# Kernel tuning notes

Hardware: AMD Instinct MI355X
Metric: run time of the kernel (lower is better)

Reference implementation:

```python
import jax, jax.numpy as jnp
import numpy as np


def setup_inputs() -> dict:
    key = jax.random.key(0)
    k1, k2, k3 = jax.random.split(key, 3)
    B, IN, OUT = 8192, 2048, 2048
    x = jax.random.normal(k1, (B, IN), dtype=jnp.float32)
    # kaiming_uniform_(a=sqrt(5)) on [OUT, IN] -> bound = sqrt(6/((1+5)*IN)) = 1/sqrt(IN)
    wb = 1.0 / np.sqrt(IN)
    weight = jax.random.uniform(k2, (OUT, IN), dtype=jnp.float32, minval=-wb, maxval=wb)
    bb = 1.0 / np.sqrt(IN)
    bias = jax.random.uniform(k3, (OUT,), dtype=jnp.float32, minval=-bb, maxval=bb)
    return {"x": x, "weight": weight, "bias": bias}


def reference(x, weight, bias):
    # out[b,o] = sum_i (x[b,i] + w[o,i]) = rowsum(x)[b] + rowsum(w)[o]
    # (identical math to the O(B*O*I) broadcast-sum, computed in O(B*I + O*I + B*O))
    x_sum = jnp.sum(x, axis=1)        # [B]
    w_sum = jnp.sum(weight, axis=1)   # [O]
    out = x_sum[:, None] + w_sum[None, :]  # [B, O]
    out = out * bias                  # note: original does `output *= self.bias`
    return out
```

## Files before the change

kernel.cpp:

```cpp
#include <hip/hip_runtime.h>


#define B_DIM 8192
#define IN_DIM 2048
#define OUT_DIM 2048

typedef float f32x4 __attribute__((ext_vector_type(4)));

__device__ __forceinline__ float butterfly_reduce(float s) {
    #pragma unroll
    for (int off = 32; off; off >>= 1)
        s += __shfl_xor(s, off, 64);
    return s;
}

__global__ __launch_bounds__(256) void wsb_kernel(const float* __restrict__ w,
                                                  const float* __restrict__ bias,
                                                  float* __restrict__ wsb) {
    const int wave = threadIdx.x >> 6;
    const int lane = threadIdx.x & 63;
    const int row  = (blockIdx.x << 2) + wave;
    const f32x4* src4 = reinterpret_cast<const f32x4*>(w + (size_t)row * IN_DIM);

    f32x4 v[8];
    #pragma unroll
    for (int k = 0; k < 8; ++k)
        v[k] = __builtin_nontemporal_load(&src4[lane + (k << 6)]);
    float s = 0.f;
    #pragma unroll
    for (int k = 0; k < 8; ++k)
        s += (v[k].x + v[k].y) + (v[k].z + v[k].w);
    s = butterfly_reduce(s);
    if (lane == 0)
        wsb[row] = s * bias[row];
}

__global__ __launch_bounds__(256) void fused_row_kernel(const float* __restrict__ x,
                                                        const float* __restrict__ bias,
                                                        const float* __restrict__ wsb,
                                                        f32x4* __restrict__ out4) {
    const int wave = threadIdx.x >> 6;
    const int lane = threadIdx.x & 63;
    const int row  = (blockIdx.x << 2) + wave;
    const f32x4* src4  = reinterpret_cast<const f32x4*>(x + (size_t)row * IN_DIM);
    const f32x4* bias4 = reinterpret_cast<const f32x4*>(bias);
    const f32x4* wsb4  = reinterpret_cast<const f32x4*>(wsb);

    f32x4 v[8];
    #pragma unroll
    for (int k = 0; k < 8; ++k)
        v[k] = __builtin_nontemporal_load(&src4[lane + (k << 6)]);
    float s = 0.f;
    #pragma unroll
    for (int k = 0; k < 8; ++k)
        s += (v[k].x + v[k].y) + (v[k].z + v[k].w);
    const float xs = butterfly_reduce(s);

    f32x4* orow = out4 + (size_t)row * (OUT_DIM / 4);
    #pragma unroll
    for (int k = 0; k < 8; ++k) {
        const int i = lane + (k << 6);
        const f32x4 bi = bias4[i];
        const f32x4 ws = wsb4[i];
        f32x4 o;
        o.x = fmaf(xs, bi.x, ws.x);
        o.y = fmaf(xs, bi.y, ws.y);
        o.z = fmaf(xs, bi.z, ws.z);
        o.w = fmaf(xs, bi.w, ws.w);
        __builtin_nontemporal_store(o, &orow[i]);
    }
}

extern "C" void kernel_launch(void* const* d_in, const int* in_sizes, int n_in,
                              void* d_out, int out_size, void* d_ws, size_t ws_size,
                              hipStream_t stream) {
    const float* x    = (const float*)d_in[0];
    const float* w    = (const float*)d_in[1];
    const float* bias = (const float*)d_in[2];
    float* out = (float*)d_out;
    float* wsb = (float*)d_ws;

    wsb_kernel<<<OUT_DIM / 4, 256, 0, stream>>>(w, bias, wsb);
    fused_row_kernel<<<B_DIM / 4, 256, 0, stream>>>(x, bias, wsb, (f32x4*)out);
}
```

Before: 32.99 us.

## Process four rows per wave with register double-buffered prefetch of next row

Each wave in the fused kernel now handles four consecutive x rows. It prefetches the next row into a second register buffer while it reduces the current row and writes that row's output, and the grid shrinks by a factor of four. The nontemporal load and store hints are also replaced with ordinary loads and stores in both kernels. The goal is to overlap load latency with compute and stores, and to reuse the bias and wsb reads. The cost is fewer waves to hide latency, more register pressure, and possibly worse cache behaviour without the nontemporal hints.

New measurement: 30.51 us. -7.5%, faster.

```diff
diff --git a/kernel.cpp b/kernel.cpp
--- a/kernel.cpp
+++ b/kernel.cpp
@@ -4,6 +4,7 @@
 #define B_DIM 8192
 #define IN_DIM 2048
 #define OUT_DIM 2048
+#define ROWS_PER_WAVE 4
 
 typedef float f32x4 __attribute__((ext_vector_type(4)));
 
@@ -14,23 +15,31 @@
     return s;
 }
 
+__device__ __forceinline__ void load_row(f32x4 (&v)[8], const float* __restrict__ row,
+                                         int lane) {
+    const f32x4* r4 = reinterpret_cast<const f32x4*>(row);
+    #pragma unroll
+    for (int k = 0; k < 8; ++k)
+        v[k] = r4[lane + (k << 6)];
+}
+
+__device__ __forceinline__ float reduce_row(const f32x4 (&v)[8]) {
+    float s = 0.f;
+    #pragma unroll
+    for (int k = 0; k < 8; ++k)
+        s += (v[k].x + v[k].y) + (v[k].z + v[k].w);
+    return butterfly_reduce(s);
+}
+
 __global__ __launch_bounds__(256) void wsb_kernel(const float* __restrict__ w,
                                                   const float* __restrict__ bias,
                                                   float* __restrict__ wsb) {
     const int wave = threadIdx.x >> 6;
     const int lane = threadIdx.x & 63;
     const int row  = (blockIdx.x << 2) + wave;
-    const f32x4* src4 = reinterpret_cast<const f32x4*>(w + (size_t)row * IN_DIM);
-
     f32x4 v[8];
-    #pragma unroll
-    for (int k = 0; k < 8; ++k)
-        v[k] = __builtin_nontemporal_load(&src4[lane + (k << 6)]);
-    float s = 0.f;
-    #pragma unroll
-    for (int k = 0; k < 8; ++k)
-        s += (v[k].x + v[k].y) + (v[k].z + v[k].w);
-    s = butterfly_reduce(s);
+    load_row(v, w + (size_t)row * IN_DIM, lane);
+    float s = reduce_row(v);
     if (lane == 0)
         wsb[row] = s * bias[row];
 }
@@ -41,33 +50,37 @@
                                                         f32x4* __restrict__ out4) {
     const int wave = threadIdx.x >> 6;
     const int lane = threadIdx.x & 63;
-    const int row  = (blockIdx.x << 2) + wave;
-    const f32x4* src4  = reinterpret_cast<const f32x4*>(x + (size_t)row * IN_DIM);
+    const int row0 = ((blockIdx.x << 2) + wave) * ROWS_PER_WAVE;
     const f32x4* bias4 = reinterpret_cast<const f32x4*>(bias);
     const f32x4* wsb4  = reinterpret_cast<const f32x4*>(wsb);
 
-    f32x4 v[8];
+    f32x4 cur[8], nxt[8];
+    load_row(cur, x + (size_t)row0 * IN_DIM, lane);
+
     #pragma unroll
-    for (int k = 0; k < 8; ++k)
-        v[k] = __builtin_nontemporal_load(&src4[lane + (k << 6)]);
-    float s = 0.f;
-    #pragma unroll
-    for (int k = 0; k < 8; ++k)
-        s += (v[k].x + v[k].y) + (v[k].z + v[k].w);
-    const float xs = butterfly_reduce(s);
+    for (int r = 0; r < ROWS_PER_WAVE; ++r) {
+        if (r + 1 < ROWS_PER_WAVE)
+            load_row(nxt, x + (size_t)(row0 + r + 1) * IN_DIM, lane);
 
-    f32x4* orow = out4 + (size_t)row * (OUT_DIM / 4);
-    #pragma unroll
-    for (int k = 0; k < 8; ++k) {
-        const int i = lane + (k << 6);
-        const f32x4 bi = bias4[i];
-        const f32x4 ws = wsb4[i];
-        f32x4 o;
-        o.x = fmaf(xs, bi.x, ws.x);
-        o.y = fmaf(xs, bi.y, ws.y);
-        o.z = fmaf(xs, bi.z, ws.z);
-        o.w = fmaf(xs, bi.w, ws.w);
-        __builtin_nontemporal_store(o, &orow[i]);
+        const float xs = reduce_row(cur);
+
+        f32x4* orow = out4 + (size_t)(row0 + r) * (OUT_DIM / 4);
+        #pragma unroll
+        for (int k = 0; k < 8; ++k) {
+            const int i = lane + (k << 6);
+            const f32x4 bi = bias4[i];
+            const f32x4 wv = wsb4[i];
+            f32x4 o;
+            o.x = fmaf(xs, bi.x, wv.x);
+            o.y = fmaf(xs, bi.y, wv.y);
+            o.z = fmaf(xs, bi.z, wv.z);
+            o.w = fmaf(xs, bi.w, wv.w);
+            orow[i] = o;
+        }
+
+        #pragma unroll
+        for (int k = 0; k < 8; ++k)
+            cur[k] = nxt[k];
     }
 }
 
@@ -81,5 +94,6 @@
     float* wsb = (float*)d_ws;
 
     wsb_kernel<<<OUT_DIM / 4, 256, 0, stream>>>(w, bias, wsb);
-    fused_row_kernel<<<B_DIM / 4, 256, 0, stream>>>(x, bias, wsb, (f32x4*)out);
+    fused_row_kernel<<<B_DIM / (4 * ROWS_PER_WAVE), 256, 0, stream>>>(x, bias, wsb,
+                                                                     (f32x4*)out);
 }
```
